# Performance work log

Measured on AMD Instinct MI355X. Metric: run time of the kernel, lower is better.

## Reference

```python
import jax, jax.numpy as jnp
import numpy as np
from jax import lax

N, T, H, E = 50000, 200, 128, 1600000


def setup_inputs() -> dict:
    key = jax.random.key(0)
    ks = jax.random.split(key, 32)
    s = 0.05
    inp = {}
    inp["lightcurve"] = jax.random.normal(ks[0], (N, T), dtype=jnp.float32)
    inp["edge_index"] = jax.random.randint(ks[1], (2, E), 0, N, dtype=jnp.int32)
    # LSTM layer 0 (input_dim=1) and layer 1 (input H), PyTorch gate order i,f,g,o
    inp["W_ih0"] = jax.random.normal(ks[2], (4 * H, 1), jnp.float32) * s
    inp["W_hh0"] = jax.random.normal(ks[3], (4 * H, H), jnp.float32) * s
    inp["b_ih0"] = jnp.zeros((4 * H,), jnp.float32)
    inp["b_hh0"] = jnp.zeros((4 * H,), jnp.float32)
    inp["W_ih1"] = jax.random.normal(ks[4], (4 * H, H), jnp.float32) * s
    inp["W_hh1"] = jax.random.normal(ks[5], (4 * H, H), jnp.float32) * s
    inp["b_ih1"] = jnp.zeros((4 * H,), jnp.float32)
    inp["b_hh1"] = jnp.zeros((4 * H,), jnp.float32)
    # 3 GCN conv layers + LayerNorms
    for i in range(3):
        inp[f"Wg{i}"] = jax.random.normal(ks[6 + i], (H, H), jnp.float32) * s
        inp[f"bg{i}"] = jnp.zeros((H,), jnp.float32)
        inp[f"gamma{i}"] = jnp.ones((H,), jnp.float32)
        inp[f"beta{i}"] = jnp.zeros((H,), jnp.float32)
    inp["W_out"] = jax.random.normal(ks[10], (H, 1), jnp.float32) * s
    inp["b_out"] = jnp.zeros((1,), jnp.float32)
    return inp


def _lstm_encode(x, W_ih0, W_hh0, b_ih0, b_hh0, W_ih1, W_hh1, b_ih1, b_hh1):
    # x: [N, T, 1] -> final hidden of layer 2: [N, H]. Both layers fused in one scan.
    n = x.shape[0]
    h = W_hh0.shape[1]

    def cell(xt, hs, cs, Wih, Whh, bih, bhh):
        g = xt @ Wih.T + hs @ Whh.T + (bih + bhh)
        i, f, gg, o = jnp.split(g, 4, axis=-1)
        cs = jax.nn.sigmoid(f) * cs + jax.nn.sigmoid(i) * jnp.tanh(gg)
        hs = jax.nn.sigmoid(o) * jnp.tanh(cs)
        return hs, cs

    def step(carry, x_t):
        h1, c1, h2, c2 = carry
        h1, c1 = cell(x_t, h1, c1, W_ih0, W_hh0, b_ih0, b_hh0)
        h2, c2 = cell(h1, h2, c2, W_ih1, W_hh1, b_ih1, b_hh1)
        return (h1, c1, h2, c2), None

    z = jnp.zeros((n, h), x.dtype)
    (_, _, h2, _), _ = lax.scan(step, (z, z, z, z), jnp.swapaxes(x, 0, 1))
    return h2


def _forward(lightcurve, W_ih0, W_hh0, b_ih0, b_hh0, W_ih1, W_hh1, b_ih1, b_hh1,
             Wg0, bg0, gamma0, beta0, Wg1, bg1, gamma1, beta1, Wg2, bg2, gamma2, beta2,
             W_out, b_out, edge_index):
    n = lightcurve.shape[0]
    h = _lstm_encode(lightcurve[..., None], W_ih0, W_hh0, b_ih0, b_hh0,
                     W_ih1, W_hh1, b_ih1, b_hh1)
    # GCN normalization (PyG GCNConv defaults: add self-loops, symmetric norm)
    loops = jnp.arange(n, dtype=edge_index.dtype)
    row = jnp.concatenate([edge_index[0], loops])  # source
    col = jnp.concatenate([edge_index[1], loops])  # target
    deg = jax.ops.segment_sum(jnp.ones_like(col, dtype=h.dtype), col, num_segments=n)
    dinv = lax.rsqrt(jnp.maximum(deg, 1.0))
    enorm = dinv[row] * dinv[col]  # [E+N]
    for Wg, bg, gm, bt in ((Wg0, bg0, gamma0, beta0), (Wg1, bg1, gamma1, beta1), (Wg2, bg2, gamma2, beta2)):
        h_prev = h
        msg = (h @ Wg)[row] * enorm[:, None]            # gather + scale
        h = jax.ops.segment_sum(msg, col, num_segments=n) + bg  # scatter-add
        mu = h.mean(-1, keepdims=True)                  # LayerNorm
        var = jnp.mean((h - mu) ** 2, axis=-1, keepdims=True)
        h = (h - mu) * lax.rsqrt(var + 1e-5) * gm + bt
        h = jax.nn.relu(h)
        h = h + h_prev  # dropout is identity in eval mode
    pooled = h.mean(axis=0, keepdims=True)  # [1, H]
    return pooled @ W_out + b_out           # [1, 1]


def reference(lightcurve, edge_index, W_ih0, W_hh0, b_ih0, b_hh0,
              W_ih1, W_hh1, b_ih1, b_hh1,
              Wg0, bg0, gamma0, beta0, Wg1, bg1, gamma1, beta1,
              Wg2, bg2, gamma2, beta2, W_out, b_out):
    return _forward(lightcurve, W_ih0, W_hh0, b_ih0, b_hh0, W_ih1, W_hh1, b_ih1, b_hh1,
                    Wg0, bg0, gamma0, beta0, Wg1, bg1, gamma1, beta1,
                    Wg2, bg2, gamma2, beta2, W_out, b_out, edge_index)
```

## Files before the change

### kernel.cpp

```cpp
#include <hip/hip_runtime.h>

#define NN 50000
#define TT 200
#define HH 128
#define EE 1600000

typedef _Float16 f16x8 __attribute__((ext_vector_type(8)));
typedef float f32x4 __attribute__((ext_vector_type(4)));

__device__ __forceinline__ float sigf(float x) {
    return __builtin_amdgcn_rcpf(1.f + __expf(-x));
}
__device__ __forceinline__ float tanhf_(float x) {
    return 1.f - 2.f * __builtin_amdgcn_rcpf(__expf(2.f * x) + 1.f);
}
__device__ __forceinline__ f32x4 sig4(f32x4 x) {
    f32x4 r; r[0] = sigf(x[0]); r[1] = sigf(x[1]); r[2] = sigf(x[2]); r[3] = sigf(x[3]); return r;
}
__device__ __forceinline__ f32x4 tanh4(f32x4 x) {
    f32x4 r; r[0] = tanhf_(x[0]); r[1] = tanhf_(x[1]); r[2] = tanhf_(x[2]); r[3] = tanhf_(x[3]); return r;
}
__device__ __forceinline__ f32x4 splat4(float s) { f32x4 r = {s, s, s, s}; return r; }
__device__ __forceinline__ unsigned short f2h_bits(float x) {
    _Float16 h = (_Float16)x;
    union { _Float16 h; unsigned short u; } cv; cv.h = h; return cv.u;
}
__device__ __forceinline__ float h2f_bits(unsigned short u) {
    union { _Float16 h; unsigned short u; } cv; cv.u = u; return (float)cv.h;
}

__global__ void pack_w(const float* __restrict__ W, unsigned short* __restrict__ out) {
    int tile = blockIdx.x;
    int jn = tile >> 2, kk = tile & 3;
    int L = threadIdx.x;
    int n = jn * 16 + (L & 15);
    int k0 = kk * 32 + (L >> 4) * 8;
    unsigned short* dst = out + (size_t)tile * 512 + L * 8;
#pragma unroll
    for (int i = 0; i < 8; ++i) dst[i] = f2h_bits(W[n * 128 + k0 + i]);
}

__global__ void bias_prep(const float* __restrict__ bih0, const float* __restrict__ bhh0,
                          const float* __restrict__ bih1, const float* __restrict__ bhh1,
                          const float* __restrict__ wih0,
                          float* __restrict__ b0g, float* __restrict__ b1g, float* __restrict__ wxg) {
    int i = blockIdx.x * 256 + threadIdx.x;
    if (i < 512) {
        b0g[i] = bih0[i] + bhh0[i];
        b1g[i] = bih1[i] + bhh1[i];
        wxg[i] = wih0[i];
    }
}

__global__ void transpose_lc(const float* __restrict__ lc, float* __restrict__ xT) {
    __shared__ float tile[32][33];
    int tx = threadIdx.x, ty = threadIdx.y;
    int n0 = blockIdx.y * 32, t0 = blockIdx.x * 32;
#pragma unroll
    for (int i = 0; i < 32; i += 8) {
        int n = n0 + ty + i, t = t0 + tx;
        if (n < NN && t < TT) tile[ty + i][tx] = lc[(size_t)n * TT + t];
    }
    __syncthreads();
#pragma unroll
    for (int i = 0; i < 32; i += 8) {
        int t = t0 + ty + i, n = n0 + tx;
        if (n < NN && t < TT) xT[(size_t)t * NN + n] = tile[tx][ty + i];
    }
}


#define MFMA16(A, B, C) __builtin_amdgcn_mfma_f32_16x16x32_f16((A), (B), (C), 0, 0, 0)

#define MMC(HB, PI, PF, PG, PO, KK) {                                          \
    f16x8 bI_ = *reinterpret_cast<const f16x8*>((PI) + (KK) * 512);            \
    f16x8 bF_ = *reinterpret_cast<const f16x8*>((PF) + (KK) * 512);            \
    f16x8 bG_ = *reinterpret_cast<const f16x8*>((PG) + (KK) * 512);            \
    f16x8 bO_ = *reinterpret_cast<const f16x8*>((PO) + (KK) * 512);            \
    f16x8 a0_ = *reinterpret_cast<const f16x8*>(&(HB)[col][(KK) * 32 + quad * 8]);      \
    f16x8 a1_ = *reinterpret_cast<const f16x8*>(&(HB)[16 + col][(KK) * 32 + quad * 8]); \
    aI0 = MFMA16(a0_, bI_, aI0); aI1 = MFMA16(a1_, bI_, aI1);                  \
    aF0 = MFMA16(a0_, bF_, aF0); aF1 = MFMA16(a1_, bF_, aF1);                  \
    aG0 = MFMA16(a0_, bG_, aG0); aG1 = MFMA16(a1_, bG_, aG1);                  \
    aO0 = MFMA16(a0_, bO_, aO0); aO1 = MFMA16(a1_, bO_, aO1);                  \
}

#define ACT0N(RT, C, H, AI, AF, AG, AO) {                                      \
    f32x4 xv_ = *reinterpret_cast<const f32x4*>(&xs[(RT) * 16 + quad * 4]);    \
    f32x4 gi_ = AI + splat4(bI) + xv_ * splat4(wI);                            \
    f32x4 gf_ = AF + splat4(bF) + xv_ * splat4(wF);                            \
    f32x4 gg_ = AG + splat4(bG) + xv_ * splat4(wG);                            \
    f32x4 go_ = AO + splat4(bO) + xv_ * splat4(wO);                            \
    C = sig4(gf_) * C + sig4(gi_) * tanh4(gg_);                                \
    H = sig4(go_) * tanh4(C);                                                  \
}

#define ACT1N(C, H, AI, AF, AG, AO) {                                          \
    f32x4 gi_ = AI + splat4(bI);                                               \
    f32x4 gf_ = AF + splat4(bF);                                               \
    f32x4 gg_ = AG + splat4(bG);                                               \
    f32x4 go_ = AO + splat4(bO);                                               \
    C = sig4(gf_) * C + sig4(gi_) * tanh4(gg_);                                \
    H = sig4(go_) * tanh4(C);                                                  \
}

#define WRH(HB, RT, H)                                                         \
    (HB)[(RT) * 16 + quad * 4 + 0][j_] = f2h_bits((H)[0]);                     \
    (HB)[(RT) * 16 + quad * 4 + 1][j_] = f2h_bits((H)[1]);                     \
    (HB)[(RT) * 16 + quad * 4 + 2][j_] = f2h_bits((H)[2]);                     \
    (HB)[(RT) * 16 + quad * 4 + 3][j_] = f2h_bits((H)[3]);

#define STEP(PB, RB, T)                                                        \
    {                      \
        f32x4 aI0 = {}, aI1 = {}, aF0 = {}, aF1 = {};                          \
        f32x4 aG0 = {}, aG1 = {}, aO0 = {}, aO1 = {};                          \
        MMC(h1s[RB], p0I, p0F, p0G, p0O, 0)                                    \
        MMC(h1s[RB], p0I, p0F, p0G, p0O, 1)                                    \
        MMC(h1s[RB], p0I, p0F, p0G, p0O, 2)                                    \
        MMC(h1s[RB], p0I, p0F, p0G, p0O, 3)                                    \
        const float bI = b0s[j_], bF = b0s[128 + j_];                          \
        const float bG = b0s[256 + j_], bO = b0s[384 + j_];                    \
        const float wI = wxs[j_], wF = wxs[128 + j_];                          \
        const float wG = wxs[256 + j_], wO = wxs[384 + j_];                    \
        f32x4 h1v0, h1v1;                                                      \
        ACT0N(0, c1_0, h1v0, aI0, aF0, aG0, aO0)                               \
        ACT0N(1, c1_1, h1v1, aI1, aF1, aG1, aO1)                               \
        WRH(h1s[PB], 0, h1v0)                                                  \
        WRH(h1s[PB], 1, h1v1)                                                  \
    }                                                                          \
    __syncthreads();                                                           \
    {             \
        f32x4 aI0 = {}, aI1 = {}, aF0 = {}, aF1 = {};                          \
        f32x4 aG0 = {}, aG1 = {}, aO0 = {}, aO1 = {};                          \
        MMC(h1s[PB], u0I, u0F, u0G, u0O, 0)                                    \
        MMC(h1s[PB], u0I, u0F, u0G, u0O, 1)                                    \
        MMC(h1s[PB], u0I, u0F, u0G, u0O, 2)                                    \
        MMC(h1s[PB], u0I, u0F, u0G, u0O, 3)                                    \
        MMC(h2s[RB], v0I, v0F, v0G, v0O, 0)                                    \
        MMC(h2s[RB], v0I, v0F, v0G, v0O, 1)                                    \
        MMC(h2s[RB], v0I, v0F, v0G, v0O, 2)                                    \
        MMC(h2s[RB], v0I, v0F, v0G, v0O, 3)                                    \
        const float bI = b1s[j_], bF = b1s[128 + j_];                          \
        const float bG = b1s[256 + j_], bO = b1s[384 + j_];                    \
        f32x4 h2v0, h2v1;                                                      \
        ACT1N(c2_0, h2v0, aI0, aF0, aG0, aO0)                                  \
        ACT1N(c2_1, h2v1, aI1, aF1, aG1, aO1)                                  \
        WRH(h2s[PB], 0, h2v0)                                                  \
        WRH(h2s[PB], 1, h2v1)                                                  \
        if (tid < 32) {                                                        \
            int n_ = n0 + tid;                                                 \
            xs[tid] = ((T) + 1 < TT && n_ < NN)                                \
                          ? xT[(size_t)((T) + 1) * NN + n_] : 0.f;             \
        }                                                                      \
    }                                                                          \
    __syncthreads();

__global__ __launch_bounds__(512, 2) void lstm_kernel(
    const float* __restrict__ xT,
    const unsigned short* __restrict__ w0p,
    const unsigned short* __restrict__ w1ip,
    const unsigned short* __restrict__ w1hp,
    const float* __restrict__ b0g, const float* __restrict__ b1g,
    const float* __restrict__ wxg,
    float* __restrict__ h2out) {
    __shared__ unsigned short h1s[2][32][136];
    __shared__ unsigned short h2s[2][32][136];
    __shared__ __align__(16) float xs[32];
    __shared__ float b0s[512], b1s[512], wxs[512];

    const int tid = threadIdx.x;
    const int w = tid >> 6;
    const int lane = tid & 63;
    const int col = lane & 15;
    const int quad = lane >> 4;
    const int n0 = blockIdx.x * 32;
    const int j_ = w * 16 + col;

    for (int i = tid; i < 2 * 32 * 136; i += 512) {
        (&h1s[0][0][0])[i] = 0; (&h2s[0][0][0])[i] = 0;
    }
    if (tid < 512) { b0s[tid] = b0g[tid]; b1s[tid] = b1g[tid]; wxs[tid] = wxg[tid]; }
    if (tid < 32) { int n = n0 + tid; xs[tid] = (n < NN) ? xT[n] : 0.f; }

    const unsigned short* p0I = w0p + (size_t)w * 2048 + lane * 8;
    const unsigned short* p0F = w0p + (size_t)(8 + w) * 2048 + lane * 8;
    const unsigned short* p0G = w0p + (size_t)(16 + w) * 2048 + lane * 8;
    const unsigned short* p0O = w0p + (size_t)(24 + w) * 2048 + lane * 8;
    const unsigned short* u0I = w1ip + (size_t)w * 2048 + lane * 8;
    const unsigned short* u0F = w1ip + (size_t)(8 + w) * 2048 + lane * 8;
    const unsigned short* u0G = w1ip + (size_t)(16 + w) * 2048 + lane * 8;
    const unsigned short* u0O = w1ip + (size_t)(24 + w) * 2048 + lane * 8;
    const unsigned short* v0I = w1hp + (size_t)w * 2048 + lane * 8;
    const unsigned short* v0F = w1hp + (size_t)(8 + w) * 2048 + lane * 8;
    const unsigned short* v0G = w1hp + (size_t)(16 + w) * 2048 + lane * 8;
    const unsigned short* v0O = w1hp + (size_t)(24 + w) * 2048 + lane * 8;

    f32x4 c1_0 = {}, c1_1 = {}, c2_0 = {}, c2_1 = {};

    __syncthreads();

#pragma unroll 1
    for (int tt = 0; tt < TT; tt += 2) {
        STEP(0, 1, tt)
        STEP(1, 0, tt + 1)
    }

    for (int i = tid; i < 32 * 128; i += 512) {
        int m = i >> 7, j = i & 127;
        int n = n0 + m;
        if (n < NN) h2out[(size_t)n * HH + j] = h2f_bits(h2s[1][m][j]);
    }
}

__global__ void deg_init(float* __restrict__ deg) {
    int i = blockIdx.x * 256 + threadIdx.x;
    if (i < NN) deg[i] = 1.f;
}
__global__ void deg_edges(const int* __restrict__ ei, float* __restrict__ deg) {
    int e = blockIdx.x * 256 + threadIdx.x;
    if (e < EE) unsafeAtomicAdd(&deg[ei[EE + e]], 1.f);
}
__global__ void dinv_k(const float* __restrict__ deg, float* __restrict__ dinv) {
    int i = blockIdx.x * 256 + threadIdx.x;
    if (i < NN) dinv[i] = rsqrtf(fmaxf(deg[i], 1.f));
}

__global__ void scan_off(const float* __restrict__ deg, int* __restrict__ off) {
    __shared__ int sp[256];
    const int tid = threadIdx.x;
    const int chunk = (NN + 255) / 256;
    const int i0 = tid * chunk;
    int s = 0;
    for (int i = 0; i < chunk; ++i) {
        int idx = i0 + i;
        if (idx < NN) s += (int)deg[idx] - 1;
    }
    sp[tid] = s;
    __syncthreads();
    for (int o = 1; o < 256; o <<= 1) {
        int v = (tid >= o) ? sp[tid - o] : 0;
        __syncthreads();
        sp[tid] += v;
        __syncthreads();
    }
    int run = sp[tid] - s;
    for (int i = 0; i < chunk; ++i) {
        int idx = i0 + i;
        if (idx < NN) { off[idx] = run; run += (int)deg[idx] - 1; }
    }
    if (tid == 255) off[NN] = sp[255];
}

__global__ void csr_fill(const int* __restrict__ ei, const float* __restrict__ dinv,
                         const int* __restrict__ off, int* __restrict__ cur,
                         int* __restrict__ crow, float* __restrict__ cw) {
    int e = blockIdx.x * 256 + threadIdx.x;
    if (e >= EE) return;
    int r = ei[e], c = ei[EE + e];
    int p = atomicAdd(&cur[c], 1);
    int idx = off[c] + p;
    crow[idx] = r;
    cw[idx] = dinv[r] * dinv[c];
}

__global__ void gcn_gemm(const float* __restrict__ h, const float* __restrict__ Wg,
                         float* __restrict__ hw) {
    __shared__ float hsT[128][36];
    int tid = threadIdx.x;
    int n0 = blockIdx.x * 32;
#pragma unroll
    for (int c = 0; c < 16; ++c) {
        int lin = c * 256 + tid;
        int m = lin >> 7, k = lin & 127;
        int n = n0 + m;
        hsT[k][m] = (n < NN) ? h[(size_t)n * HH + k] : 0.f;
    }
    __syncthreads();
    int j = tid & 127, p = tid >> 7;
    float acc[16];
#pragma unroll
    for (int m = 0; m < 16; ++m) acc[m] = 0.f;
    for (int k = 0; k < 128; ++k) {
        float wg = Wg[k * 128 + j];
        const float4* hp = reinterpret_cast<const float4*>(&hsT[k][p * 16]);
        float4 a = hp[0], b = hp[1], c = hp[2], d = hp[3];
        acc[0]  += a.x * wg; acc[1]  += a.y * wg; acc[2]  += a.z * wg; acc[3]  += a.w * wg;
        acc[4]  += b.x * wg; acc[5]  += b.y * wg; acc[6]  += b.z * wg; acc[7]  += b.w * wg;
        acc[8]  += c.x * wg; acc[9]  += c.y * wg; acc[10] += c.z * wg; acc[11] += c.w * wg;
        acc[12] += d.x * wg; acc[13] += d.y * wg; acc[14] += d.z * wg; acc[15] += d.w * wg;
    }
#pragma unroll
    for (int m = 0; m < 16; ++m) {
        int n = n0 + p * 16 + m;
        if (n < NN) hw[(size_t)n * HH + j] = acc[m];
    }
}

__global__ __launch_bounds__(256) void gcn_agg(
    const float* __restrict__ hw, const int* __restrict__ off,
    const int* __restrict__ crow, const float* __restrict__ cw,
    const float* __restrict__ dinv, const float* __restrict__ bg,
    const float* __restrict__ gamma, const float* __restrict__ beta,
    float* __restrict__ h) {
    __shared__ float xch[4][2];
    const int tid = threadIdx.x;
    const int half = tid >> 7;
    const int f = tid & 127;
    const int v = blockIdx.x * 2 + half;
    const float d = dinv[v];
    float acc = bg[f] + d * d * hw[v * HH + f];
    const int s1 = off[v + 1];
    for (int s = off[v]; s < s1; ++s) {
        int r = crow[s];
        float wv = cw[s];
        acc = fmaf(wv, hw[r * HH + f], acc);
    }
    float sum = acc, sq = acc * acc;
#pragma unroll
    for (int o = 32; o; o >>= 1) { sum += __shfl_xor(sum, o); sq += __shfl_xor(sq, o); }
    int wid = tid >> 6;
    if ((tid & 63) == 0) { xch[wid][0] = sum; xch[wid][1] = sq; }
    __syncthreads();
    sum += xch[wid ^ 1][0]; sq += xch[wid ^ 1][1];
    float mu = sum * (1.f / 128.f);
    float var = sq * (1.f / 128.f) - mu * mu;
    float rn = rsqrtf(var + 1e-5f);
    float o = (acc - mu) * rn * gamma[f] + beta[f];
    h[v * HH + f] = fmaxf(o, 0.f) + h[v * HH + f];
}

__global__ void pool_k(const float* __restrict__ h, float* __restrict__ pooled) {
    int j = threadIdx.x & 127, p = threadIdx.x >> 7;
    float s = 0.f;
    for (int n = blockIdx.x * 2 + p; n < NN; n += 512) s += h[(size_t)n * HH + j];
    unsafeAtomicAdd(&pooled[j], s);
}

__global__ void final_k(const float* __restrict__ pooled, const float* __restrict__ Wout,
                        const float* __restrict__ bout, float* __restrict__ out) {
    int lane = threadIdx.x;
    float s = pooled[lane] * Wout[lane] + pooled[lane + 64] * Wout[lane + 64];
#pragma unroll
    for (int o = 32; o; o >>= 1) s += __shfl_xor(s, o);
    if (lane == 0) out[0] = s * (1.f / (float)NN) + bout[0];
}

extern "C" void kernel_launch(void* const* d_in, const int* in_sizes, int n_in,
                              void* d_out, int out_size, void* d_ws, size_t ws_size,
                              hipStream_t stream) {
    const float* lc   = (const float*)d_in[0];
    const int*   ei   = (const int*)d_in[1];
    const float* Wih0 = (const float*)d_in[2];
    const float* Whh0 = (const float*)d_in[3];
    const float* bih0 = (const float*)d_in[4];
    const float* bhh0 = (const float*)d_in[5];
    const float* Wih1 = (const float*)d_in[6];
    const float* Whh1 = (const float*)d_in[7];
    const float* bih1 = (const float*)d_in[8];
    const float* bhh1 = (const float*)d_in[9];
    const float* Wout = (const float*)d_in[22];
    const float* bout = (const float*)d_in[23];
    float* out = (float*)d_out;

    float* ws   = (float*)d_ws;
    float* h    = ws;
    float* hw   = ws + 6400000;
    float* xT   = ws + 6400000;
    int*   off  = (int*)(ws + 12800000);
    int*   cur  = off + 50048;
    int*   crow = cur + 50048;
    float* cw   = (float*)(crow + EE);
    float* P      = ws + 16400064;
    float* deg    = P;
    float* dinv   = deg + 50000;
    float* b0g    = dinv + 50000;
    float* b1g    = b0g + 512;
    float* wxg    = b1g + 512;
    float* pooled = wxg + 512;
    unsigned short* w0p  = (unsigned short*)(pooled + 128);
    unsigned short* w1ip = w0p + 65536;
    unsigned short* w1hp = w1ip + 65536;

    pack_w<<<128, 64, 0, stream>>>(Whh0, w0p);
    pack_w<<<128, 64, 0, stream>>>(Wih1, w1ip);
    pack_w<<<128, 64, 0, stream>>>(Whh1, w1hp);
    bias_prep<<<2, 256, 0, stream>>>(bih0, bhh0, bih1, bhh1, Wih0, b0g, b1g, wxg);
    {
        dim3 g((TT + 31) / 32, (NN + 31) / 32), b(32, 8);
        transpose_lc<<<g, b, 0, stream>>>(lc, xT);
    }
    deg_init<<<(NN + 255) / 256, 256, 0, stream>>>(deg);
    deg_edges<<<(EE + 255) / 256, 256, 0, stream>>>(ei, deg);
    dinv_k<<<(NN + 255) / 256, 256, 0, stream>>>(deg, dinv);

    lstm_kernel<<<(NN + 31) / 32, 512, 0, stream>>>(xT, w0p, w1ip, w1hp, b0g, b1g, wxg, h);

    hipMemsetAsync(cur, 0, 50000 * sizeof(int), stream);
    scan_off<<<1, 256, 0, stream>>>(deg, off);
    csr_fill<<<(EE + 255) / 256, 256, 0, stream>>>(ei, dinv, off, cur, crow, cw);

    for (int l = 0; l < 3; ++l) {
        const float* Wg = (const float*)d_in[10 + 4 * l];
        const float* bg = (const float*)d_in[11 + 4 * l];
        const float* gm = (const float*)d_in[12 + 4 * l];
        const float* bt = (const float*)d_in[13 + 4 * l];
        gcn_gemm<<<(NN + 31) / 32, 256, 0, stream>>>(h, Wg, hw);
        gcn_agg<<<NN / 2, 256, 0, stream>>>(hw, off, crow, cw, dinv, bg, gm, bt, h);
    }

    hipMemsetAsync(pooled, 0, HH * sizeof(float), stream);
    pool_k<<<256, 256, 0, stream>>>(h, pooled);
    final_k<<<1, 64, 0, stream>>>(pooled, Wout, bout, out);
}
```

Before: 7.906 ms.

## Skew LSTM layers into one barrier per step and fold exp scaling into weights

The two LSTM layers are software-pipelined: in each interval, layer-2 step t and layer-1 step t+1 both read the same h1 buffer, so only one __syncthreads per timestep is needed instead of two. A prologue computes layer-1 step 0 before the loop. Activation constants (-log2e for sigmoid gates, 2log2e for the tanh gate) are folded into the packed weights and biases so the kernel can call exp2 directly, with s_setprio wrapping the MFMA blocks and launch bounds raised to 4 waves per SIMD. The changes risk register pressure from the higher occupancy target and slight fp16 rounding differences from the pre-scaled weights.

New measurement: 23.29 ms. +194.5%, slower.

```diff
diff --git a/kernel.cpp b/kernel.cpp
--- a/kernel.cpp
+++ b/kernel.cpp
@@ -5,20 +5,23 @@
 #define HH 128
 #define EE 1600000
 
+#define NL2E  -1.4426950408889634f
+#define TWOL2E 2.8853900817779268f
+
 typedef _Float16 f16x8 __attribute__((ext_vector_type(8)));
 typedef float f32x4 __attribute__((ext_vector_type(4)));
 
-__device__ __forceinline__ float sigf(float x) {
-    return __builtin_amdgcn_rcpf(1.f + __expf(-x));
-}
-__device__ __forceinline__ float tanhf_(float x) {
-    return 1.f - 2.f * __builtin_amdgcn_rcpf(__expf(2.f * x) + 1.f);
-}
-__device__ __forceinline__ f32x4 sig4(f32x4 x) {
-    f32x4 r; r[0] = sigf(x[0]); r[1] = sigf(x[1]); r[2] = sigf(x[2]); r[3] = sigf(x[3]); return r;
-}
-__device__ __forceinline__ f32x4 tanh4(f32x4 x) {
-    f32x4 r; r[0] = tanhf_(x[0]); r[1] = tanhf_(x[1]); r[2] = tanhf_(x[2]); r[3] = tanhf_(x[3]); return r;
+__device__ __forceinline__ float sg2(float x) {
+    return __builtin_amdgcn_rcpf(1.f + exp2f(x));
+}
+__device__ __forceinline__ float th2(float x) {
+    return 1.f - 2.f * __builtin_amdgcn_rcpf(exp2f(x) + 1.f);
+}
+__device__ __forceinline__ f32x4 sg2_4(f32x4 x) {
+    f32x4 r; r[0] = sg2(x[0]); r[1] = sg2(x[1]); r[2] = sg2(x[2]); r[3] = sg2(x[3]); return r;
+}
+__device__ __forceinline__ f32x4 th2_4(f32x4 x) {
+    f32x4 r; r[0] = th2(x[0]); r[1] = th2(x[1]); r[2] = th2(x[2]); r[3] = th2(x[3]); return r;
 }
 __device__ __forceinline__ f32x4 splat4(float s) { f32x4 r = {s, s, s, s}; return r; }
 __device__ __forceinline__ unsigned short f2h_bits(float x) {
@@ -35,9 +38,10 @@
     int L = threadIdx.x;
     int n = jn * 16 + (L & 15);
     int k0 = kk * 32 + (L >> 4) * 8;
+    float sc = ((jn >> 3) == 2) ? TWOL2E : NL2E;
     unsigned short* dst = out + (size_t)tile * 512 + L * 8;
 #pragma unroll
-    for (int i = 0; i < 8; ++i) dst[i] = f2h_bits(W[n * 128 + k0 + i]);
+    for (int i = 0; i < 8; ++i) dst[i] = f2h_bits(W[n * 128 + k0 + i] * sc);
 }
 
 __global__ void bias_prep(const float* __restrict__ bih0, const float* __restrict__ bhh0,
@@ -46,9 +50,10 @@
                           float* __restrict__ b0g, float* __restrict__ b1g, float* __restrict__ wxg) {
     int i = blockIdx.x * 256 + threadIdx.x;
     if (i < 512) {
-        b0g[i] = bih0[i] + bhh0[i];
-        b1g[i] = bih1[i] + bhh1[i];
-        wxg[i] = wih0[i];
+        float sc = ((i >> 7) == 2) ? TWOL2E : NL2E;
+        b0g[i] = (bih0[i] + bhh0[i]) * sc;
+        b1g[i] = (bih1[i] + bhh1[i]) * sc;
+        wxg[i] = wih0[i] * sc;
     }
 }
 
@@ -85,14 +90,14 @@
     aO0 = MFMA16(a0_, bO_, aO0); aO1 = MFMA16(a1_, bO_, aO1);                  \
 }
 
-#define ACT0N(RT, C, H, AI, AF, AG, AO) {                                      \
-    f32x4 xv_ = *reinterpret_cast<const f32x4*>(&xs[(RT) * 16 + quad * 4]);    \
+#define ACT0N(RT, C, H, AI, AF, AG, AO, XP) {                                  \
+    f32x4 xv_ = *reinterpret_cast<const f32x4*>(&xb[XP][(RT) * 16 + quad * 4]);\
     f32x4 gi_ = AI + splat4(bI) + xv_ * splat4(wI);                            \
     f32x4 gf_ = AF + splat4(bF) + xv_ * splat4(wF);                            \
     f32x4 gg_ = AG + splat4(bG) + xv_ * splat4(wG);                            \
     f32x4 go_ = AO + splat4(bO) + xv_ * splat4(wO);                            \
-    C = sig4(gf_) * C + sig4(gi_) * tanh4(gg_);                                \
-    H = sig4(go_) * tanh4(C);                                                  \
+    C = sg2_4(gf_) * C + sg2_4(gi_) * th2_4(gg_);                              \
+    H = sg2_4(go_) * th2_4(C * splat4(TWOL2E));                                \
 }
 
 #define ACT1N(C, H, AI, AF, AG, AO) {                                          \
@@ -100,8 +105,8 @@
     f32x4 gf_ = AF + splat4(bF);                                               \
     f32x4 gg_ = AG + splat4(bG);                                               \
     f32x4 go_ = AO + splat4(bO);                                               \
-    C = sig4(gf_) * C + sig4(gi_) * tanh4(gg_);                                \
-    H = sig4(go_) * tanh4(C);                                                  \
+    C = sg2_4(gf_) * C + sg2_4(gi_) * th2_4(gg_);                              \
+    H = sg2_4(go_) * th2_4(C * splat4(TWOL2E));                                \
 }
 
 #define WRH(HB, RT, H)                                                         \
@@ -110,52 +115,55 @@
     (HB)[(RT) * 16 + quad * 4 + 2][j_] = f2h_bits((H)[2]);                     \
     (HB)[(RT) * 16 + quad * 4 + 3][j_] = f2h_bits((H)[3]);
 
-#define STEP(PB, RB, T)                                                        \
-    {                      \
+#define INTERVAL(P, KX)                                                        \
+    {            \
         f32x4 aI0 = {}, aI1 = {}, aF0 = {}, aF1 = {};                          \
         f32x4 aG0 = {}, aG1 = {}, aO0 = {}, aO1 = {};                          \
-        MMC(h1s[RB], p0I, p0F, p0G, p0O, 0)                                    \
-        MMC(h1s[RB], p0I, p0F, p0G, p0O, 1)                                    \
-        MMC(h1s[RB], p0I, p0F, p0G, p0O, 2)                                    \
-        MMC(h1s[RB], p0I, p0F, p0G, p0O, 3)                                    \
+        __builtin_amdgcn_s_setprio(1);                                         \
+        MMC(h1s[P], u0I, u0F, u0G, u0O, 0)                                     \
+        MMC(h1s[P], u0I, u0F, u0G, u0O, 1)                                     \
+        MMC(h1s[P], u0I, u0F, u0G, u0O, 2)                                     \
+        MMC(h1s[P], u0I, u0F, u0G, u0O, 3)                                     \
+        MMC(h2s[(P) ^ 1], v0I, v0F, v0G, v0O, 0)                               \
+        MMC(h2s[(P) ^ 1], v0I, v0F, v0G, v0O, 1)                               \
+        MMC(h2s[(P) ^ 1], v0I, v0F, v0G, v0O, 2)                               \
+        MMC(h2s[(P) ^ 1], v0I, v0F, v0G, v0O, 3)                               \
+        __builtin_amdgcn_s_setprio(0);                                         \
+        if (tid < 32) {                   \
+            int n_ = n0 + tid;                                                 \
+            xb[(P)][tid] = ((KX) + 2 < TT && n_ < NN)                          \
+                               ? xT[(size_t)((KX) + 2) * NN + n_] : 0.f;       \
+        }                                                                      \
+        const float bI = b1s[j_], bF = b1s[128 + j_];                          \
+        const float bG = b1s[256 + j_], bO = b1s[384 + j_];                    \
+        f32x4 h2v0, h2v1;                                                      \
+        ACT1N(c2_0, h2v0, aI0, aF0, aG0, aO0)                                  \
+        ACT1N(c2_1, h2v1, aI1, aF1, aG1, aO1)                                  \
+        WRH(h2s[P], 0, h2v0)                                                   \
+        WRH(h2s[P], 1, h2v1)                                                   \
+    }                                                                          \
+    {           \
+        f32x4 aI0 = {}, aI1 = {}, aF0 = {}, aF1 = {};                          \
+        f32x4 aG0 = {}, aG1 = {}, aO0 = {}, aO1 = {};                          \
+        __builtin_amdgcn_s_setprio(1);                                         \
+        MMC(h1s[P], p0I, p0F, p0G, p0O, 0)                                     \
+        MMC(h1s[P], p0I, p0F, p0G, p0O, 1)                                     \
+        MMC(h1s[P], p0I, p0F, p0G, p0O, 2)                                     \
+        MMC(h1s[P], p0I, p0F, p0G, p0O, 3)                                     \
+        __builtin_amdgcn_s_setprio(0);                                         \
         const float bI = b0s[j_], bF = b0s[128 + j_];                          \
         const float bG = b0s[256 + j_], bO = b0s[384 + j_];                    \
         const float wI = wxs[j_], wF = wxs[128 + j_];                          \
         const float wG = wxs[256 + j_], wO = wxs[384 + j_];                    \
         f32x4 h1v0, h1v1;                                                      \
-        ACT0N(0, c1_0, h1v0, aI0, aF0, aG0, aO0)                               \
-        ACT0N(1, c1_1, h1v1, aI1, aF1, aG1, aO1)                               \
-        WRH(h1s[PB], 0, h1v0)                                                  \
-        WRH(h1s[PB], 1, h1v1)                                                  \
+        ACT0N(0, c1_0, h1v0, aI0, aF0, aG0, aO0, (P) ^ 1)                      \
+        ACT0N(1, c1_1, h1v1, aI1, aF1, aG1, aO1, (P) ^ 1)                      \
+        WRH(h1s[(P) ^ 1], 0, h1v0)                                             \
+        WRH(h1s[(P) ^ 1], 1, h1v1)                                             \
     }                                                                          \
-    __syncthreads();                                                           \
-    {             \
-        f32x4 aI0 = {}, aI1 = {}, aF0 = {}, aF1 = {};                          \
-        f32x4 aG0 = {}, aG1 = {}, aO0 = {}, aO1 = {};                          \
-        MMC(h1s[PB], u0I, u0F, u0G, u0O, 0)                                    \
-        MMC(h1s[PB], u0I, u0F, u0G, u0O, 1)                                    \
-        MMC(h1s[PB], u0I, u0F, u0G, u0O, 2)                                    \
-        MMC(h1s[PB], u0I, u0F, u0G, u0O, 3)                                    \
-        MMC(h2s[RB], v0I, v0F, v0G, v0O, 0)                                    \
-        MMC(h2s[RB], v0I, v0F, v0G, v0O, 1)                                    \
-        MMC(h2s[RB], v0I, v0F, v0G, v0O, 2)                                    \
-        MMC(h2s[RB], v0I, v0F, v0G, v0O, 3)                                    \
-        const float bI = b1s[j_], bF = b1s[128 + j_];                          \
-        const float bG = b1s[256 + j_], bO = b1s[384 + j_];                    \
-        f32x4 h2v0, h2v1;                                                      \
-        ACT1N(c2_0, h2v0, aI0, aF0, aG0, aO0)                                  \
-        ACT1N(c2_1, h2v1, aI1, aF1, aG1, aO1)                                  \
-        WRH(h2s[PB], 0, h2v0)                                                  \
-        WRH(h2s[PB], 1, h2v1)                                                  \
-        if (tid < 32) {                                                        \
-            int n_ = n0 + tid;                                                 \
-            xs[tid] = ((T) + 1 < TT && n_ < NN)                                \
-                          ? xT[(size_t)((T) + 1) * NN + n_] : 0.f;             \
-        }                                                                      \
-    }                                                                          \
-    __syncthreads();
-
-__global__ __launch_bounds__(512, 2) void lstm_kernel(
+    __syncthreads();
+
+__global__ __launch_bounds__(512, 4) void lstm_kernel(
     const float* __restrict__ xT,
     const unsigned short* __restrict__ w0p,
     const unsigned short* __restrict__ w1ip,
@@ -165,7 +173,7 @@
     float* __restrict__ h2out) {
     __shared__ unsigned short h1s[2][32][136];
     __shared__ unsigned short h2s[2][32][136];
-    __shared__ __align__(16) float xs[32];
+    __shared__ __align__(16) float xb[2][32];
     __shared__ float b0s[512], b1s[512], wxs[512];
 
     const int tid = threadIdx.x;
@@ -176,11 +184,13 @@
     const int n0 = blockIdx.x * 32;
     const int j_ = w * 16 + col;
 
-    for (int i = tid; i < 2 * 32 * 136; i += 512) {
-        (&h1s[0][0][0])[i] = 0; (&h2s[0][0][0])[i] = 0;
-    }
-    if (tid < 512) { b0s[tid] = b0g[tid]; b1s[tid] = b1g[tid]; wxs[tid] = wxg[tid]; }
-    if (tid < 32) { int n = n0 + tid; xs[tid] = (n < NN) ? xT[n] : 0.f; }
+    for (int i = tid; i < 2 * 32 * 136; i += 512) (&h2s[0][0][0])[i] = 0;
+    b0s[tid] = b0g[tid]; b1s[tid] = b1g[tid]; wxs[tid] = wxg[tid];
+    if (tid < 32) {
+        int n = n0 + tid;
+        xb[0][tid] = (n < NN) ? xT[n] : 0.f;
+        xb[1][tid] = (n < NN) ? xT[NN + n] : 0.f;
+    }
 
     const unsigned short* p0I = w0p + (size_t)w * 2048 + lane * 8;
     const unsigned short* p0F = w0p + (size_t)(8 + w) * 2048 + lane * 8;
@@ -199,10 +209,38 @@
 
     __syncthreads();
 
+    {
+        const float bI = b0s[j_], bF = b0s[128 + j_];
+        const float bG = b0s[256 + j_], bO = b0s[384 + j_];
+        const float wI = wxs[j_], wF = wxs[128 + j_];
+        const float wG = wxs[256 + j_], wO = wxs[384 + j_];
+        (void)bF; (void)wF;
+        f32x4 h1v0, h1v1;
+        {
+            f32x4 xv = *reinterpret_cast<const f32x4*>(&xb[0][quad * 4]);
+            f32x4 gi = splat4(bI) + xv * splat4(wI);
+            f32x4 gg = splat4(bG) + xv * splat4(wG);
+            f32x4 go = splat4(bO) + xv * splat4(wO);
+            c1_0 = sg2_4(gi) * th2_4(gg);
+            h1v0 = sg2_4(go) * th2_4(c1_0 * splat4(TWOL2E));
+        }
+        {
+            f32x4 xv = *reinterpret_cast<const f32x4*>(&xb[0][16 + quad * 4]);
+            f32x4 gi = splat4(bI) + xv * splat4(wI);
+            f32x4 gg = splat4(bG) + xv * splat4(wG);
+            f32x4 go = splat4(bO) + xv * splat4(wO);
+            c1_1 = sg2_4(gi) * th2_4(gg);
+            h1v1 = sg2_4(go) * th2_4(c1_1 * splat4(TWOL2E));
+        }
+        WRH(h1s[0], 0, h1v0)
+        WRH(h1s[0], 1, h1v1)
+    }
+    __syncthreads();
+
 #pragma unroll 1
-    for (int tt = 0; tt < TT; tt += 2) {
-        STEP(0, 1, tt)
-        STEP(1, 0, tt + 1)
+    for (int k = 0; k < TT; k += 2) {
+        INTERVAL(0, k)
+        INTERVAL(1, k + 1)
     }
 
     for (int i = tid; i < 32 * 128; i += 512) {
```

## Keep LSTM weights register-resident, prescale gates for exp2, pad LDS stride

Applied to the files above, without the earlier changes.

The 48 f16x8 weight fragments per wave are loaded once into registers before the time loop, replacing per-step global/L2 loads of the weights. Weights and biases are prescaled by -log2e (2·log2e for the g gate) so the sigmoid and tanh use exp2 directly, dropping a multiply per activation. The LDS row stride is padded from 136 to 152 to change bank mapping, and the next-step x load is issued earlier to overlap with the activations. Holding weights in registers uses about 192 VGPRs per lane, which risks spills or lower occupancy under launch_bounds(512,2), and the f16 prescaling slightly changes rounding.

Result: slower. 9.447 ms (+19.5%).

```diff
diff --git a/kernel.cpp b/kernel.cpp
--- a/kernel.cpp
+++ b/kernel.cpp
@@ -5,20 +5,25 @@
 #define HH 128
 #define EE 1600000
 
+#define NL2E  -1.4426950408889634f
+#define TWOL2E 2.8853900817779268f
+
+#define STR 152
+
 typedef _Float16 f16x8 __attribute__((ext_vector_type(8)));
 typedef float f32x4 __attribute__((ext_vector_type(4)));
 
-__device__ __forceinline__ float sigf(float x) {
-    return __builtin_amdgcn_rcpf(1.f + __expf(-x));
-}
-__device__ __forceinline__ float tanhf_(float x) {
-    return 1.f - 2.f * __builtin_amdgcn_rcpf(__expf(2.f * x) + 1.f);
-}
-__device__ __forceinline__ f32x4 sig4(f32x4 x) {
-    f32x4 r; r[0] = sigf(x[0]); r[1] = sigf(x[1]); r[2] = sigf(x[2]); r[3] = sigf(x[3]); return r;
-}
-__device__ __forceinline__ f32x4 tanh4(f32x4 x) {
-    f32x4 r; r[0] = tanhf_(x[0]); r[1] = tanhf_(x[1]); r[2] = tanhf_(x[2]); r[3] = tanhf_(x[3]); return r;
+__device__ __forceinline__ float sg2(float x) {
+    return __builtin_amdgcn_rcpf(1.f + exp2f(x));
+}
+__device__ __forceinline__ float th2(float x) {
+    return 1.f - 2.f * __builtin_amdgcn_rcpf(exp2f(x) + 1.f);
+}
+__device__ __forceinline__ f32x4 sg2_4(f32x4 x) {
+    f32x4 r; r[0] = sg2(x[0]); r[1] = sg2(x[1]); r[2] = sg2(x[2]); r[3] = sg2(x[3]); return r;
+}
+__device__ __forceinline__ f32x4 th2_4(f32x4 x) {
+    f32x4 r; r[0] = th2(x[0]); r[1] = th2(x[1]); r[2] = th2(x[2]); r[3] = th2(x[3]); return r;
 }
 __device__ __forceinline__ f32x4 splat4(float s) { f32x4 r = {s, s, s, s}; return r; }
 __device__ __forceinline__ unsigned short f2h_bits(float x) {
@@ -35,9 +40,10 @@
     int L = threadIdx.x;
     int n = jn * 16 + (L & 15);
     int k0 = kk * 32 + (L >> 4) * 8;
+    float sc = ((jn >> 3) == 2) ? TWOL2E : NL2E;
     unsigned short* dst = out + (size_t)tile * 512 + L * 8;
 #pragma unroll
-    for (int i = 0; i < 8; ++i) dst[i] = f2h_bits(W[n * 128 + k0 + i]);
+    for (int i = 0; i < 8; ++i) dst[i] = f2h_bits(W[n * 128 + k0 + i] * sc);
 }
 
 __global__ void bias_prep(const float* __restrict__ bih0, const float* __restrict__ bhh0,
@@ -46,9 +52,10 @@
                           float* __restrict__ b0g, float* __restrict__ b1g, float* __restrict__ wxg) {
     int i = blockIdx.x * 256 + threadIdx.x;
     if (i < 512) {
-        b0g[i] = bih0[i] + bhh0[i];
-        b1g[i] = bih1[i] + bhh1[i];
-        wxg[i] = wih0[i];
+        float sc = ((i >> 7) == 2) ? TWOL2E : NL2E;
+        b0g[i] = (bih0[i] + bhh0[i]) * sc;
+        b1g[i] = (bih1[i] + bhh1[i]) * sc;
+        wxg[i] = wih0[i] * sc;
     }
 }
 
@@ -72,17 +79,16 @@
 
 #define MFMA16(A, B, C) __builtin_amdgcn_mfma_f32_16x16x32_f16((A), (B), (C), 0, 0, 0)
 
-#define MMC(HB, PI, PF, PG, PO, KK) {                                          \
-    f16x8 bI_ = *reinterpret_cast<const f16x8*>((PI) + (KK) * 512);            \
-    f16x8 bF_ = *reinterpret_cast<const f16x8*>((PF) + (KK) * 512);            \
-    f16x8 bG_ = *reinterpret_cast<const f16x8*>((PG) + (KK) * 512);            \
-    f16x8 bO_ = *reinterpret_cast<const f16x8*>((PO) + (KK) * 512);            \
+#define LDW(V, BASE, G, KK) \
+    const f16x8 V = *reinterpret_cast<const f16x8*>((BASE) + (size_t)((G) * 8 + w) * 2048 + (KK) * 512 + lane * 8);
+
+#define MMCR(HB, BI, BF, BG, BO, KK) {                                         \
     f16x8 a0_ = *reinterpret_cast<const f16x8*>(&(HB)[col][(KK) * 32 + quad * 8]);      \
     f16x8 a1_ = *reinterpret_cast<const f16x8*>(&(HB)[16 + col][(KK) * 32 + quad * 8]); \
-    aI0 = MFMA16(a0_, bI_, aI0); aI1 = MFMA16(a1_, bI_, aI1);                  \
-    aF0 = MFMA16(a0_, bF_, aF0); aF1 = MFMA16(a1_, bF_, aF1);                  \
-    aG0 = MFMA16(a0_, bG_, aG0); aG1 = MFMA16(a1_, bG_, aG1);                  \
-    aO0 = MFMA16(a0_, bO_, aO0); aO1 = MFMA16(a1_, bO_, aO1);                  \
+    aI0 = MFMA16(a0_, BI, aI0); aI1 = MFMA16(a1_, BI, aI1);                    \
+    aF0 = MFMA16(a0_, BF, aF0); aF1 = MFMA16(a1_, BF, aF1);                    \
+    aG0 = MFMA16(a0_, BG, aG0); aG1 = MFMA16(a1_, BG, aG1);                    \
+    aO0 = MFMA16(a0_, BO, aO0); aO1 = MFMA16(a1_, BO, aO1);                    \
 }
 
 #define ACT0N(RT, C, H, AI, AF, AG, AO) {                                      \
@@ -91,8 +97,8 @@
     f32x4 gf_ = AF + splat4(bF) + xv_ * splat4(wF);                            \
     f32x4 gg_ = AG + splat4(bG) + xv_ * splat4(wG);                            \
     f32x4 go_ = AO + splat4(bO) + xv_ * splat4(wO);                            \
-    C = sig4(gf_) * C + sig4(gi_) * tanh4(gg_);                                \
-    H = sig4(go_) * tanh4(C);                                                  \
+    C = sg2_4(gf_) * C + sg2_4(gi_) * th2_4(gg_);                              \
+    H = sg2_4(go_) * th2_4(C * splat4(TWOL2E));                                \
 }
 
 #define ACT1N(C, H, AI, AF, AG, AO) {                                          \
@@ -100,8 +106,8 @@
     f32x4 gf_ = AF + splat4(bF);                                               \
     f32x4 gg_ = AG + splat4(bG);                                               \
     f32x4 go_ = AO + splat4(bO);                                               \
-    C = sig4(gf_) * C + sig4(gi_) * tanh4(gg_);                                \
-    H = sig4(go_) * tanh4(C);                                                  \
+    C = sg2_4(gf_) * C + sg2_4(gi_) * th2_4(gg_);                              \
+    H = sg2_4(go_) * th2_4(C * splat4(TWOL2E));                                \
 }
 
 #define WRH(HB, RT, H)                                                         \
@@ -114,10 +120,10 @@
     {                      \
         f32x4 aI0 = {}, aI1 = {}, aF0 = {}, aF1 = {};                          \
         f32x4 aG0 = {}, aG1 = {}, aO0 = {}, aO1 = {};                          \
-        MMC(h1s[RB], p0I, p0F, p0G, p0O, 0)                                    \
-        MMC(h1s[RB], p0I, p0F, p0G, p0O, 1)                                    \
-        MMC(h1s[RB], p0I, p0F, p0G, p0O, 2)                                    \
-        MMC(h1s[RB], p0I, p0F, p0G, p0O, 3)                                    \
+        MMCR(h1s[RB], pI0, pF0, pG0, pO0, 0)                                   \
+        MMCR(h1s[RB], pI1, pF1, pG1, pO1, 1)                                   \
+        MMCR(h1s[RB], pI2, pF2, pG2, pO2, 2)                                   \
+        MMCR(h1s[RB], pI3, pF3, pG3, pO3, 3)                                   \
         const float bI = b0s[j_], bF = b0s[128 + j_];                          \
         const float bG = b0s[256 + j_], bO = b0s[384 + j_];                    \
         const float wI = wxs[j_], wF = wxs[128 + j_];                          \
@@ -132,14 +138,19 @@
     {             \
         f32x4 aI0 = {}, aI1 = {}, aF0 = {}, aF1 = {};                          \
         f32x4 aG0 = {}, aG1 = {}, aO0 = {}, aO1 = {};                          \
-        MMC(h1s[PB], u0I, u0F, u0G, u0O, 0)                                    \
-        MMC(h1s[PB], u0I, u0F, u0G, u0O, 1)                                    \
-        MMC(h1s[PB], u0I, u0F, u0G, u0O, 2)                                    \
-        MMC(h1s[PB], u0I, u0F, u0G, u0O, 3)                                    \
-        MMC(h2s[RB], v0I, v0F, v0G, v0O, 0)                                    \
-        MMC(h2s[RB], v0I, v0F, v0G, v0O, 1)                                    \
-        MMC(h2s[RB], v0I, v0F, v0G, v0O, 2)                                    \
-        MMC(h2s[RB], v0I, v0F, v0G, v0O, 3)                                    \
+        MMCR(h1s[PB], uI0, uF0, uG0, uO0, 0)                                   \
+        MMCR(h1s[PB], uI1, uF1, uG1, uO1, 1)                                   \
+        MMCR(h1s[PB], uI2, uF2, uG2, uO2, 2)                                   \
+        MMCR(h1s[PB], uI3, uF3, uG3, uO3, 3)                                   \
+        MMCR(h2s[RB], vI0, vF0, vG0, vO0, 0)                                   \
+        MMCR(h2s[RB], vI1, vF1, vG1, vO1, 1)                                   \
+        MMCR(h2s[RB], vI2, vF2, vG2, vO2, 2)                                   \
+        MMCR(h2s[RB], vI3, vF3, vG3, vO3, 3)                                   \
+        if (tid < 32) {                    \
+            int n_ = n0 + tid;                                                 \
+            xs[tid] = ((T) + 1 < TT && n_ < NN)                                \
+                          ? xT[(size_t)((T) + 1) * NN + n_] : 0.f;             \
+        }                                                                      \
         const float bI = b1s[j_], bF = b1s[128 + j_];                          \
         const float bG = b1s[256 + j_], bO = b1s[384 + j_];                    \
         f32x4 h2v0, h2v1;                                                      \
@@ -147,11 +158,6 @@
         ACT1N(c2_1, h2v1, aI1, aF1, aG1, aO1)                                  \
         WRH(h2s[PB], 0, h2v0)                                                  \
         WRH(h2s[PB], 1, h2v1)                                                  \
-        if (tid < 32) {                                                        \
-            int n_ = n0 + tid;                                                 \
-            xs[tid] = ((T) + 1 < TT && n_ < NN)                                \
-                          ? xT[(size_t)((T) + 1) * NN + n_] : 0.f;             \
-        }                                                                      \
     }                                                                          \
     __syncthreads();
 
@@ -163,8 +169,8 @@
     const float* __restrict__ b0g, const float* __restrict__ b1g,
     const float* __restrict__ wxg,
     float* __restrict__ h2out) {
-    __shared__ unsigned short h1s[2][32][136];
-    __shared__ unsigned short h2s[2][32][136];
+    __shared__ unsigned short h1s[2][32][STR];
+    __shared__ unsigned short h2s[2][32][STR];
     __shared__ __align__(16) float xs[32];
     __shared__ float b0s[512], b1s[512], wxs[512];
 
@@ -176,24 +182,24 @@
     const int n0 = blockIdx.x * 32;
     const int j_ = w * 16 + col;
 
-    for (int i = tid; i < 2 * 32 * 136; i += 512) {
+    for (int i = tid; i < 2 * 32 * STR; i += 512) {
         (&h1s[0][0][0])[i] = 0; (&h2s[0][0][0])[i] = 0;
     }
-    if (tid < 512) { b0s[tid] = b0g[tid]; b1s[tid] = b1g[tid]; wxs[tid] = wxg[tid]; }
+    b0s[tid] = b0g[tid]; b1s[tid] = b1g[tid]; wxs[tid] = wxg[tid];
     if (tid < 32) { int n = n0 + tid; xs[tid] = (n < NN) ? xT[n] : 0.f; }
 
-    const unsigned short* p0I = w0p + (size_t)w * 2048 + lane * 8;
-    const unsigned short* p0F = w0p + (size_t)(8 + w) * 2048 + lane * 8;
-    const unsigned short* p0G = w0p + (size_t)(16 + w) * 2048 + lane * 8;
-    const unsigned short* p0O = w0p + (size_t)(24 + w) * 2048 + lane * 8;
-    const unsigned short* u0I = w1ip + (size_t)w * 2048 + lane * 8;
-    const unsigned short* u0F = w1ip + (size_t)(8 + w) * 2048 + lane * 8;
-    const unsigned short* u0G = w1ip + (size_t)(16 + w) * 2048 + lane * 8;
-    const unsigned short* u0O = w1ip + (size_t)(24 + w) * 2048 + lane * 8;
-    const unsigned short* v0I = w1hp + (size_t)w * 2048 + lane * 8;
-    const unsigned short* v0F = w1hp + (size_t)(8 + w) * 2048 + lane * 8;
-    const unsigned short* v0G = w1hp + (size_t)(16 + w) * 2048 + lane * 8;
-    const unsigned short* v0O = w1hp + (size_t)(24 + w) * 2048 + lane * 8;
+    LDW(pI0, w0p, 0, 0) LDW(pI1, w0p, 0, 1) LDW(pI2, w0p, 0, 2) LDW(pI3, w0p, 0, 3)
+    LDW(pF0, w0p, 1, 0) LDW(pF1, w0p, 1, 1) LDW(pF2, w0p, 1, 2) LDW(pF3, w0p, 1, 3)
+    LDW(pG0, w0p, 2, 0) LDW(pG1, w0p, 2, 1) LDW(pG2, w0p, 2, 2) LDW(pG3, w0p, 2, 3)
+    LDW(pO0, w0p, 3, 0) LDW(pO1, w0p, 3, 1) LDW(pO2, w0p, 3, 2) LDW(pO3, w0p, 3, 3)
+    LDW(uI0, w1ip, 0, 0) LDW(uI1, w1ip, 0, 1) LDW(uI2, w1ip, 0, 2) LDW(uI3, w1ip, 0, 3)
+    LDW(uF0, w1ip, 1, 0) LDW(uF1, w1ip, 1, 1) LDW(uF2, w1ip, 1, 2) LDW(uF3, w1ip, 1, 3)
+    LDW(uG0, w1ip, 2, 0) LDW(uG1, w1ip, 2, 1) LDW(uG2, w1ip, 2, 2) LDW(uG3, w1ip, 2, 3)
+    LDW(uO0, w1ip, 3, 0) LDW(uO1, w1ip, 3, 1) LDW(uO2, w1ip, 3, 2) LDW(uO3, w1ip, 3, 3)
+    LDW(vI0, w1hp, 0, 0) LDW(vI1, w1hp, 0, 1) LDW(vI2, w1hp, 0, 2) LDW(vI3, w1hp, 0, 3)
+    LDW(vF0, w1hp, 1, 0) LDW(vF1, w1hp, 1, 1) LDW(vF2, w1hp, 1, 2) LDW(vF3, w1hp, 1, 3)
+    LDW(vG0, w1hp, 2, 0) LDW(vG1, w1hp, 2, 1) LDW(vG2, w1hp, 2, 2) LDW(vG3, w1hp, 2, 3)
+    LDW(vO0, w1hp, 3, 0) LDW(vO1, w1hp, 3, 1) LDW(vO2, w1hp, 3, 2) LDW(vO3, w1hp, 3, 3)
 
     f32x4 c1_0 = {}, c1_1 = {}, c2_0 = {}, c2_1 = {};
 
```
